# Kernel tuning notes

Measured on AMD Instinct MI355X. Metric: run time of the kernel, lower is better.

The kernel has to match this reference:

```python
import jax, jax.numpy as jnp
import numpy as np

EPS = 1e-8


def normalize_points(p):
    # p: [..., D+1]; normalize feature part to unit L2 norm, fix sign by last coord
    f = p[..., :-1]
    h = p[..., -1:]
    zero_mask = jnp.all(f == 0, axis=-1, keepdims=True)
    f = jnp.where(zero_mask, jnp.ones_like(f), f)
    norm = jnp.linalg.norm(f, axis=-1, keepdims=True)
    nf = f / jnp.clip(norm, EPS)
    n = jnp.concatenate([nf, h], axis=-1)
    sign = jnp.sign(n[..., -1:])
    sign = jnp.where(sign == 0, jnp.ones_like(sign), sign)
    return n * sign


def uhg_transform(x, weight):
    # x: [M, D_in+1], weight: [D_out, D_in]
    f = x[..., :-1]
    h = x[..., -1:]
    t = jnp.matmul(f, weight.T)  # [M, D_out]
    norm = jnp.linalg.norm(t, axis=-1, keepdims=True)
    t = t / jnp.clip(norm, EPS)
    return normalize_points(jnp.concatenate([t, h], axis=-1))


def setup_inputs() -> dict:
    key = jax.random.key(0)
    k1, k2, k3, k4 = jax.random.split(key, 4)
    N, E = 20000, 320000
    D_IN, D_OUT = 256, 256  # in_features-1, out_features
    x = jax.random.normal(k1, (N, D_IN + 1), dtype=jnp.float32)
    edge_index = jax.random.randint(k2, (2, E), 0, N, dtype=jnp.int32)
    # orthogonal-ish init approximated by row-normalized gaussian weights
    W_self = jax.random.normal(k3, (D_OUT, D_IN), dtype=jnp.float32)
    W_self = W_self / jnp.clip(jnp.linalg.norm(W_self, axis=1, keepdims=True), EPS)
    W_neigh = jax.random.normal(k4, (D_OUT, D_IN), dtype=jnp.float32)
    W_neigh = W_neigh / jnp.clip(jnp.linalg.norm(W_neigh, axis=1, keepdims=True), EPS)
    return {"x": x, "W_self": W_self, "W_neigh": W_neigh, "edge_index": edge_index}


def reference(x, W_self, W_neigh, edge_index):
    N = x.shape[0]
    D_OUT = W_self.shape[0]
    x = normalize_points(x)
    row, col = edge_index[0], edge_index[1]

    self_trans = uhg_transform(x, W_self)              # [N, D_OUT+1]
    neigh_trans = uhg_transform(x[col], W_neigh)       # [E, D_OUT+1]

    # mean aggregation: scatter-add full (features + homogeneous), count-divide features only
    out = jnp.zeros((N, D_OUT + 1), dtype=x.dtype).at[:, -1].set(1.0)
    out = out.at[row].add(neigh_trans)
    count = jnp.zeros((N, 1), dtype=x.dtype).at[row].add(1.0)
    count = jnp.clip(count, 1.0)
    out = jnp.concatenate([out[:, :-1] / count, out[:, -1:]], axis=-1)
    out = normalize_points(out)

    # uhg_weighted_average(p1, p2, 0.5): elementwise blend then renormalize
    t = jnp.clip(0.5 / (1.0 - 0.5 + EPS), EPS, 1e8)
    p1 = normalize_points(self_trans)
    p2 = normalize_points(out)
    avg = (p1 * t + p2) / jnp.clip(t + 1.0, EPS)
    combined = normalize_points(avg)
    return normalize_points(combined)
```

## Files before the change

kernel.cpp:

```cpp
#include <hip/hip_runtime.h>
#include <hip/hip_bf16.h>

#define EPSF 1e-8f
#define CAP 64

typedef __attribute__((ext_vector_type(4))) float floatx4;
typedef __attribute__((ext_vector_type(2))) float floatx2;
typedef __attribute__((ext_vector_type(2))) long longx2;

__device__ inline unsigned short f2bf(float v) {
    union { float f; unsigned int u; } un; un.f = v;
    unsigned int r = (un.u + 0x7fffu + ((un.u >> 16) & 1u)) >> 16;
    return (unsigned short)r;
}
__device__ inline float bf2f(unsigned short u) {
    union { unsigned int i; float f; } un; un.i = ((unsigned int)u) << 16;
    return un.f;
}

__device__ inline unsigned char f2fp8(float v) {
#if __has_builtin(__builtin_amdgcn_cvt_pk_fp8_f32)
    return (unsigned char)(__builtin_amdgcn_cvt_pk_fp8_f32(v, 0.f, 0u, false) & 0xff);
#else
    union { float f; unsigned u; } x; x.f = v;
    unsigned s = x.u >> 31; x.u &= 0x7fffffffu;
    if (x.f != x.f || x.f == 0.f) return (unsigned char)(s << 7);
    int e = (int)((x.u >> 23) & 0xff) - 127 + 7;
    unsigned m = x.u & 0x7fffffu;
    unsigned char r;
    if (e >= 1) {
        unsigned keep = m >> 20, rest = m & 0xfffffu;
        keep += (rest > 0x80000u) || (rest == 0x80000u && (keep & 1));
        if (keep == 8) { keep = 0; e += 1; }
        if (e > 15) { e = 15; keep = 6; }
        r = (unsigned char)((e << 3) | keep);
    } else {
        int q = (int)(x.f * 512.f + 0.5f);
        if (q > 7) r = 0x08; else r = (unsigned char)q;
    }
    return (unsigned char)(r | (s << 7));
#endif
}
__device__ inline unsigned pk_fp8x4(float v0, float v1, float v2, float v3) {
#if __has_builtin(__builtin_amdgcn_cvt_pk_fp8_f32)
    unsigned u = __builtin_amdgcn_cvt_pk_fp8_f32(v0, v1, 0u, false);
    u = __builtin_amdgcn_cvt_pk_fp8_f32(v2, v3, u, true);
    return u;
#else
    return (unsigned)f2fp8(v0) | ((unsigned)f2fp8(v1) << 8)
         | ((unsigned)f2fp8(v2) << 16) | ((unsigned)f2fp8(v3) << 24);
#endif
}
__device__ inline floatx2 fp8x2_to_f32(unsigned int u, bool word) {
#if __has_builtin(__builtin_amdgcn_cvt_pk_f32_fp8)
    return word ? __builtin_amdgcn_cvt_pk_f32_fp8(u, true)
                : __builtin_amdgcn_cvt_pk_f32_fp8(u, false);
#else
    floatx2 out;
    #pragma unroll
    for (int i = 0; i < 2; ++i) {
        unsigned char b = (u >> ((word ? 16 : 0) + 8 * i)) & 0xff;
        unsigned s = (b >> 7) & 1, e = (b >> 3) & 15, m = b & 7;
        float v;
        if (e) { union { unsigned u2; float f; } x; x.u2 = (s << 31) | ((e + 120u) << 23) | (m << 20); v = x.f; }
        else   { v = (s ? -1.f : 1.f) * (float)m * 0.001953125f; }
        out[i] = v;
    }
    return out;
#endif
}

__device__ inline void acc16(float* acc, uint4 u) {
    floatx2 p;
    p = fp8x2_to_f32(u.x, false); acc[0]  += p[0]; acc[1]  += p[1];
    p = fp8x2_to_f32(u.x, true);  acc[2]  += p[0]; acc[3]  += p[1];
    p = fp8x2_to_f32(u.y, false); acc[4]  += p[0]; acc[5]  += p[1];
    p = fp8x2_to_f32(u.y, true);  acc[6]  += p[0]; acc[7]  += p[1];
    p = fp8x2_to_f32(u.z, false); acc[8]  += p[0]; acc[9]  += p[1];
    p = fp8x2_to_f32(u.z, true);  acc[10] += p[0]; acc[11] += p[1];
    p = fp8x2_to_f32(u.w, false); acc[12] += p[0]; acc[13] += p[1];
    p = fp8x2_to_f32(u.w, true);  acc[14] += p[0]; acc[15] += p[1];
}

__global__ __launch_bounds__(512) void k_front(
        const float* __restrict__ x, const float* __restrict__ Ws,
        const float* __restrict__ Wn,
        unsigned char* __restrict__ Wswz,
        float* __restrict__ xh, int* __restrict__ cnt, int N) {
    int b = blockIdx.x, t = threadIdx.x;
    if (b < 32) {
        int idx = b * 512 + t;
        int t0 = (idx & 3) * 4;
        int lane = (idx >> 2) & 63;
        int p = (idx >> 8) & 3;
        int g = (idx >> 10) & 3;
        int wq = (idx >> 12) & 3;
        int q = lane >> 4, l16 = lane & 15;
        int row = wq * 64 + g * 16 + l16;
        int s = 2 * p + (t0 >> 3);
        int k0 = 32 * s + 8 * q + (t0 & 7);
        float4 vs = *reinterpret_cast<const float4*>(Ws + row * 256 + k0);
        float4 vn = *reinterpret_cast<const float4*>(Wn + row * 256 + k0);
        reinterpret_cast<unsigned*>(Wswz)[idx] = pk_fp8x4(vs.x, vs.y, vs.z, vs.w);
        reinterpret_cast<unsigned*>(Wswz)[16384 + idx] = pk_fp8x4(vn.x, vn.y, vn.z, vn.w);
    } else {
        int i = (b - 32) * 512 + t;
        if (i < N) {
            xh[i] = fabsf(x[(size_t)i * 257 + 256]);
            cnt[i] = 0;
        }
    }
}

__global__ __launch_bounds__(512, 8) void k_mid(
        const float* __restrict__ x,
        const unsigned char* __restrict__ Wswz,
        const int* __restrict__ ei,
        int* __restrict__ cnt, int* __restrict__ scol,
        unsigned short* __restrict__ selfb, unsigned char* __restrict__ yb8,
        int N, int E, int EB) {
    __shared__ __align__(16) unsigned char As[32][256];
    __shared__ __align__(16) unsigned short sOut[32][256];
    __shared__ float pss[8][32];
    __shared__ float sgnS[32];
    int b = blockIdx.x, tid = threadIdx.x;
    int T = gridDim.x;

    int ebBefore = (int)(((long)b * EB) / T);
    bool isBucket = ((int)(((long)(b + 1) * EB) / T)) != ebBefore;
    if (isBucket) {
        int e = ebBefore * 512 + tid;
        if (e < E) {
            int r = ei[e], c = ei[E + e];
            int pos = atomicAdd(&cnt[r], 1);
            if (pos < CAP) scol[r * CAP + pos] = c;
        }
        return;
    }

    int wave = tid >> 6, lane = tid & 63;
    int quad = lane >> 4, l16 = lane & 15;
    int mat = wave >> 2, wq = wave & 3;
    int row0 = (b - ebBefore) * 32;

    if (tid < 32) {
        int gr = row0 + tid; if (gr >= N) gr = N - 1;
        float h = x[(size_t)gr * 257 + 256];
        sgnS[tid] = (h < 0.f) ? -1.f : 1.f;
    }
    __syncthreads();

    #pragma unroll
    for (int ps = 0; ps < 4; ++ps) {
        int c = ps * 512 + tid;
        int row = c >> 6, k0 = (c & 63) * 4;
        int gr = row0 + row; if (gr >= N) gr = N - 1;
        float4 v = *reinterpret_cast<const float4*>(x + (size_t)gr * 257 + k0);
        float sg = sgnS[row];
        int s = k0 >> 5, q = (k0 >> 3) & 3, j0 = k0 & 7;
        int dst = (q * 64 + (s >> 1) * 16 + (s & 1) * 8 + j0 + row * 16) & 255;
        *reinterpret_cast<unsigned*>(&As[row][dst]) =
            pk_fp8x4(v.x * sg, v.y * sg, v.z * sg, v.w * sg);
    }
    __syncthreads();

    const unsigned char* Wb = Wswz + ((size_t)mat << 16) + ((size_t)wq << 14);
    int rowA = l16, rowB = 16 + l16;

    floatx4 acc[2][4];
    #pragma unroll
    for (int rt = 0; rt < 2; ++rt)
        #pragma unroll
        for (int g = 0; g < 4; ++g) acc[rt][g] = floatx4{0.f, 0.f, 0.f, 0.f};

    #pragma unroll
    for (int p = 0; p < 4; ++p) {
        longx2 a0 = *reinterpret_cast<const longx2*>(
            &As[rowA][(quad * 64 + p * 16 + rowA * 16) & 255]);
        longx2 a1 = *reinterpret_cast<const longx2*>(
            &As[rowB][(quad * 64 + p * 16 + rowB * 16) & 255]);
        #pragma unroll
        for (int g = 0; g < 4; ++g) {
            longx2 w = *reinterpret_cast<const longx2*>(
                Wb + (((g * 4 + p) * 64 + lane) << 4));
            acc[0][g] = __builtin_amdgcn_mfma_f32_16x16x32_fp8_fp8(a0[0], w[0], acc[0][g], 0, 0, 0);
            acc[1][g] = __builtin_amdgcn_mfma_f32_16x16x32_fp8_fp8(a1[0], w[0], acc[1][g], 0, 0, 0);
            acc[0][g] = __builtin_amdgcn_mfma_f32_16x16x32_fp8_fp8(a0[1], w[1], acc[0][g], 0, 0, 0);
            acc[1][g] = __builtin_amdgcn_mfma_f32_16x16x32_fp8_fp8(a1[1], w[1], acc[1][g], 0, 0, 0);
        }
    }

    #pragma unroll
    for (int rt = 0; rt < 2; ++rt) {
        float s[4];
        #pragma unroll
        for (int reg = 0; reg < 4; ++reg) {
            float v = 0.f;
            #pragma unroll
            for (int g = 0; g < 4; ++g) v += acc[rt][g][reg] * acc[rt][g][reg];
            #pragma unroll
            for (int o = 8; o > 0; o >>= 1) v += __shfl_down(v, o, 64);
            s[reg] = v;
        }
        if (l16 == 0) {
            #pragma unroll
            for (int reg = 0; reg < 4; ++reg)
                pss[wave][rt * 16 + quad * 4 + reg] = s[reg];
        }
    }
    __syncthreads();

    int wb = mat * 4;
    #pragma unroll
    for (int rt = 0; rt < 2; ++rt)
        #pragma unroll
        for (int reg = 0; reg < 4; ++reg) {
            int r32 = rt * 16 + quad * 4 + reg;
            float ss = pss[wb][r32] + pss[wb + 1][r32]
                     + pss[wb + 2][r32] + pss[wb + 3][r32];
            bool zero = (ss == 0.f);
            float scale = zero ? 0.f : (1.f / fmaxf(sqrtf(ss), EPSF));
            int xb = ((r32 >> 2) & 3) << 4;
            #pragma unroll
            for (int g = 0; g < 4; ++g) {
                int col = wq * 64 + 16 * g + l16;
                float val = zero ? 0.0625f : acc[rt][g][reg] * scale;
                int cs = col ^ xb;
                if (mat == 0) sOut[r32][cs] = f2bf(val);
                else          As[r32][cs]   = f2fp8(val);
            }
        }
    __syncthreads();

    {
        int r = tid >> 4;
        int gr = row0 + r;
        if (gr < N) {
            int blk = (tid & 15) ^ ((r >> 2) & 3);
            int cb  = blk * 16;
            int cbo = (tid & 15) * 16;
            uint4 a0 = *reinterpret_cast<const uint4*>(&sOut[r][cb]);
            uint4 a1 = *reinterpret_cast<const uint4*>(&sOut[r][cb + 8]);
            *reinterpret_cast<uint4*>(selfb + (size_t)gr * 256 + cbo) = a0;
            *reinterpret_cast<uint4*>(selfb + (size_t)gr * 256 + cbo + 8) = a1;
            uint4 y0 = *reinterpret_cast<const uint4*>(&As[r][cb]);
            *reinterpret_cast<uint4*>(yb8 + (size_t)gr * 256 + cbo) = y0;
        }
    }
}

__global__ __launch_bounds__(256) void k_agg_combine(
        const int* __restrict__ cnt, const int* __restrict__ scol,
        const unsigned char* __restrict__ yb8,
        const float* __restrict__ xh,
        const unsigned short* __restrict__ selfb,
        float* __restrict__ out, int N) {
    int wid = (blockIdx.x * 256 + threadIdx.x) >> 6;
    if (wid >= N) return;
    int lane = threadIdx.x & 63;
    int g = lane >> 4, l16 = lane & 15;
    int deg = cnt[wid]; if (deg > CAP) deg = CAP;
    int beg = wid * CAP;

    float acc[16];
    #pragma unroll
    for (int j = 0; j < 16; ++j) acc[j] = 0.f;

    int e = 0;
    for (; e + 8 <= deg; e += 8) {
        int c0 = scol[beg + e + g];
        int c1 = scol[beg + e + 4 + g];
        uint4 u0 = *reinterpret_cast<const uint4*>(yb8 + (size_t)c0 * 256 + l16 * 16);
        uint4 u1 = *reinterpret_cast<const uint4*>(yb8 + (size_t)c1 * 256 + l16 * 16);
        acc16(acc, u0);
        acc16(acc, u1);
    }
    if (e < deg) {
        int i0 = e + g;
        if (i0 < deg) {
            int c = scol[beg + i0];
            uint4 u = *reinterpret_cast<const uint4*>(yb8 + (size_t)c * 256 + l16 * 16);
            acc16(acc, u);
        }
        int i1 = e + 4 + g;
        if (i1 < deg) {
            int c = scol[beg + i1];
            uint4 u = *reinterpret_cast<const uint4*>(yb8 + (size_t)c * 256 + l16 * 16);
            acc16(acc, u);
        }
    }
    #pragma unroll
    for (int j = 0; j < 16; ++j) {
        acc[j] += __shfl_xor(acc[j], 16, 64);
        acc[j] += __shfl_xor(acc[j], 32, 64);
    }

    float hs = 0.f;
    for (int j = lane; j < deg; j += 64) hs += xh[scol[beg + j]];
    #pragma unroll
    for (int o = 32; o > 0; o >>= 1) hs += __shfl_xor(hs, o, 64);

    float cn = (deg > 0) ? (float)deg : 1.f;
    float rcn = 1.f / cn;
    float m_[16];
    float ss = 0.f;
    #pragma unroll
    for (int j = 0; j < 16; ++j) { m_[j] = acc[j] * rcn; ss += m_[j] * m_[j]; }
    #pragma unroll
    for (int o = 1; o < 16; o <<= 1) ss += __shfl_xor(ss, o, 64);
    bool z = (ss == 0.f);
    float inv = 1.f / fmaxf(z ? 16.f : sqrtf(ss), EPSF);

    const unsigned short* sp = selfb + (size_t)wid * 256 + l16 * 16;
    uint4 s0 = *reinterpret_cast<const uint4*>(sp);
    uint4 s1 = *reinterpret_cast<const uint4*>(sp + 8);
    unsigned sw[8] = { s0.x, s0.y, s0.z, s0.w, s1.x, s1.y, s1.z, s1.w };
    float v_[16];
    float ss2 = 0.f;
    #pragma unroll
    for (int j = 0; j < 8; ++j) {
        float slo = bf2f((unsigned short)(sw[j] & 0xffff));
        float shi = bf2f((unsigned short)(sw[j] >> 16));
        float olo = (z ? 1.f : m_[2 * j]) * inv;
        float ohi = (z ? 1.f : m_[2 * j + 1]) * inv;
        v_[2 * j]     = 0.5f * (slo + olo);
        v_[2 * j + 1] = 0.5f * (shi + ohi);
        ss2 += v_[2 * j] * v_[2 * j] + v_[2 * j + 1] * v_[2 * j + 1];
    }
    #pragma unroll
    for (int o = 1; o < 16; o <<= 1) ss2 += __shfl_xor(ss2, o, 64);
    bool z2 = (ss2 == 0.f);
    float inv2 = 1.f / fmaxf(z2 ? 16.f : sqrtf(ss2), EPSF);

    if (g == 0) {
        float* op = out + (size_t)wid * 257 + l16 * 16;
        #pragma unroll
        for (int j = 0; j < 16; ++j) op[j] = (z2 ? 1.f : v_[j]) * inv2;
    }
    if (lane == 0) out[(size_t)wid * 257 + 256] = 0.5f * (xh[wid] + 1.f + hs);
}

extern "C" void kernel_launch(void* const* d_in, const int* in_sizes, int n_in,
                              void* d_out, int out_size, void* d_ws, size_t ws_size,
                              hipStream_t stream) {
    const float* x  = (const float*)d_in[0];
    const float* Ws = (const float*)d_in[1];
    const float* Wn = (const float*)d_in[2];
    const int*   ei = (const int*)d_in[3];
    int N = in_sizes[0] / 257;
    int E = in_sizes[3] / 2;
    float* out = (float*)d_out;

    char* ws = (char*)d_ws;
    size_t off = 0;
    auto alloc = [&](size_t bytes) {
        void* p = ws + off;
        off = (off + bytes + 255) & ~(size_t)255;
        return p;
    };
    unsigned char* Wswz = (unsigned char*)alloc(131072);
    float* xh    = (float*)alloc((size_t)N * 4);
    unsigned char* yb8 = (unsigned char*)alloc((size_t)N * 256);
    unsigned short* selfb = (unsigned short*)alloc((size_t)N * 256 * 2);
    int* cnt  = (int*)alloc((size_t)N * 4);
    int* scol = (int*)alloc((size_t)N * CAP * 4);

    int XB = (N + 511) / 512;
    hipLaunchKernelGGL(k_front, dim3(32 + XB), dim3(512), 0, stream,
                       x, Ws, Wn, Wswz, xh, cnt, N);
    int GB = (N + 31) / 32, EB = (E + 511) / 512;
    hipLaunchKernelGGL(k_mid, dim3(GB + EB), dim3(512), 0, stream,
                       x, Wswz, ei, cnt, scol, selfb, yb8, N, E, EB);
    hipLaunchKernelGGL(k_agg_combine, dim3((N + 3) / 4), dim3(256), 0, stream,
                       cnt, scol, yb8, xh, selfb, out, N);
}
```

Baseline: 125.6 us.

## Fuse three kernels into one persistent kernel with software grid barriers

```diff
diff --git a/kernel.cpp b/kernel.cpp
--- a/kernel.cpp
+++ b/kernel.cpp
@@ -3,6 +3,7 @@
 
 #define EPSF 1e-8f
 #define CAP 64
+#define NBLK 512
 
 typedef __attribute__((ext_vector_type(4))) float floatx4;
 typedef __attribute__((ext_vector_type(2))) float floatx2;
@@ -82,262 +83,272 @@
     p = fp8x2_to_f32(u.w, true);  acc[14] += p[0]; acc[15] += p[1];
 }
 
-__global__ __launch_bounds__(512) void k_front(
+__device__ inline void swbar(unsigned* bar, unsigned target) {
+    __syncthreads();
+    if (threadIdx.x == 0) {
+        __threadfence();
+        atomicAdd(bar, 1u);
+        long guard = 0;
+        while (atomicAdd(bar, 0u) < target) {
+            __builtin_amdgcn_s_sleep(8);
+            if (++guard > (1L << 22)) break;
+        }
+        __threadfence();
+    }
+    __syncthreads();
+}
+
+__global__ __launch_bounds__(512, 4) void k_fused(
         const float* __restrict__ x, const float* __restrict__ Ws,
-        const float* __restrict__ Wn,
-        unsigned char* __restrict__ Wswz,
-        float* __restrict__ xh, int* __restrict__ cnt, int N) {
-    int b = blockIdx.x, t = threadIdx.x;
-    if (b < 32) {
-        int idx = b * 512 + t;
-        int t0 = (idx & 3) * 4;
-        int lane = (idx >> 2) & 63;
-        int p = (idx >> 8) & 3;
-        int g = (idx >> 10) & 3;
-        int wq = (idx >> 12) & 3;
-        int q = lane >> 4, l16 = lane & 15;
-        int row = wq * 64 + g * 16 + l16;
-        int s = 2 * p + (t0 >> 3);
-        int k0 = 32 * s + 8 * q + (t0 & 7);
-        float4 vs = *reinterpret_cast<const float4*>(Ws + row * 256 + k0);
-        float4 vn = *reinterpret_cast<const float4*>(Wn + row * 256 + k0);
-        reinterpret_cast<unsigned*>(Wswz)[idx] = pk_fp8x4(vs.x, vs.y, vs.z, vs.w);
-        reinterpret_cast<unsigned*>(Wswz)[16384 + idx] = pk_fp8x4(vn.x, vn.y, vn.z, vn.w);
-    } else {
-        int i = (b - 32) * 512 + t;
-        if (i < N) {
-            xh[i] = fabsf(x[(size_t)i * 257 + 256]);
-            cnt[i] = 0;
-        }
-    }
-}
-
-__global__ __launch_bounds__(512, 8) void k_mid(
-        const float* __restrict__ x,
-        const unsigned char* __restrict__ Wswz,
-        const int* __restrict__ ei,
-        int* __restrict__ cnt, int* __restrict__ scol,
+        const float* __restrict__ Wn, const int* __restrict__ ei,
+        unsigned char* __restrict__ Wswz, float* __restrict__ xh,
+        int* __restrict__ cnt, unsigned* __restrict__ bar,
+        int* __restrict__ scol,
         unsigned short* __restrict__ selfb, unsigned char* __restrict__ yb8,
-        int N, int E, int EB) {
+        float* __restrict__ out, int N, int E) {
     __shared__ __align__(16) unsigned char As[32][256];
     __shared__ __align__(16) unsigned short sOut[32][256];
     __shared__ float pss[8][32];
     __shared__ float sgnS[32];
-    int b = blockIdx.x, tid = threadIdx.x;
-    int T = gridDim.x;
-
-    int ebBefore = (int)(((long)b * EB) / T);
-    bool isBucket = ((int)(((long)(b + 1) * EB) / T)) != ebBefore;
-    if (isBucket) {
-        int e = ebBefore * 512 + tid;
-        if (e < E) {
-            int r = ei[e], c = ei[E + e];
-            int pos = atomicAdd(&cnt[r], 1);
-            if (pos < CAP) scol[r * CAP + pos] = c;
-        }
-        return;
-    }
-
+
+    int b0 = blockIdx.x, tid = threadIdx.x;
     int wave = tid >> 6, lane = tid & 63;
     int quad = lane >> 4, l16 = lane & 15;
-    int mat = wave >> 2, wq = wave & 3;
-    int row0 = (b - ebBefore) * 32;
-
-    if (tid < 32) {
-        int gr = row0 + tid; if (gr >= N) gr = N - 1;
-        float h = x[(size_t)gr * 257 + 256];
-        sgnS[tid] = (h < 0.f) ? -1.f : 1.f;
-    }
-    __syncthreads();
-
-    #pragma unroll
-    for (int ps = 0; ps < 4; ++ps) {
-        int c = ps * 512 + tid;
-        int row = c >> 6, k0 = (c & 63) * 4;
-        int gr = row0 + row; if (gr >= N) gr = N - 1;
-        float4 v = *reinterpret_cast<const float4*>(x + (size_t)gr * 257 + k0);
-        float sg = sgnS[row];
-        int s = k0 >> 5, q = (k0 >> 3) & 3, j0 = k0 & 7;
-        int dst = (q * 64 + (s >> 1) * 16 + (s & 1) * 8 + j0 + row * 16) & 255;
-        *reinterpret_cast<unsigned*>(&As[row][dst]) =
-            pk_fp8x4(v.x * sg, v.y * sg, v.z * sg, v.w * sg);
-    }
-    __syncthreads();
-
-    const unsigned char* Wb = Wswz + ((size_t)mat << 16) + ((size_t)wq << 14);
-    int rowA = l16, rowB = 16 + l16;
-
-    floatx4 acc[2][4];
-    #pragma unroll
-    for (int rt = 0; rt < 2; ++rt)
-        #pragma unroll
-        for (int g = 0; g < 4; ++g) acc[rt][g] = floatx4{0.f, 0.f, 0.f, 0.f};
-
-    #pragma unroll
-    for (int p = 0; p < 4; ++p) {
-        longx2 a0 = *reinterpret_cast<const longx2*>(
-            &As[rowA][(quad * 64 + p * 16 + rowA * 16) & 255]);
-        longx2 a1 = *reinterpret_cast<const longx2*>(
-            &As[rowB][(quad * 64 + p * 16 + rowB * 16) & 255]);
-        #pragma unroll
-        for (int g = 0; g < 4; ++g) {
-            longx2 w = *reinterpret_cast<const longx2*>(
-                Wb + (((g * 4 + p) * 64 + lane) << 4));
-            acc[0][g] = __builtin_amdgcn_mfma_f32_16x16x32_fp8_fp8(a0[0], w[0], acc[0][g], 0, 0, 0);
-            acc[1][g] = __builtin_amdgcn_mfma_f32_16x16x32_fp8_fp8(a1[0], w[0], acc[1][g], 0, 0, 0);
-            acc[0][g] = __builtin_amdgcn_mfma_f32_16x16x32_fp8_fp8(a0[1], w[1], acc[0][g], 0, 0, 0);
-            acc[1][g] = __builtin_amdgcn_mfma_f32_16x16x32_fp8_fp8(a1[1], w[1], acc[1][g], 0, 0, 0);
-        }
-    }
-
-    #pragma unroll
-    for (int rt = 0; rt < 2; ++rt) {
-        float s[4];
-        #pragma unroll
-        for (int reg = 0; reg < 4; ++reg) {
-            float v = 0.f;
-            #pragma unroll
-            for (int g = 0; g < 4; ++g) v += acc[rt][g][reg] * acc[rt][g][reg];
-            #pragma unroll
-            for (int o = 8; o > 0; o >>= 1) v += __shfl_down(v, o, 64);
-            s[reg] = v;
-        }
-        if (l16 == 0) {
-            #pragma unroll
-            for (int reg = 0; reg < 4; ++reg)
-                pss[wave][rt * 16 + quad * 4 + reg] = s[reg];
-        }
-    }
-    __syncthreads();
-
-    int wb = mat * 4;
-    #pragma unroll
-    for (int rt = 0; rt < 2; ++rt)
-        #pragma unroll
-        for (int reg = 0; reg < 4; ++reg) {
-            int r32 = rt * 16 + quad * 4 + reg;
-            float ss = pss[wb][r32] + pss[wb + 1][r32]
-                     + pss[wb + 2][r32] + pss[wb + 3][r32];
-            bool zero = (ss == 0.f);
-            float scale = zero ? 0.f : (1.f / fmaxf(sqrtf(ss), EPSF));
-            int xb = ((r32 >> 2) & 3) << 4;
-            #pragma unroll
-            for (int g = 0; g < 4; ++g) {
-                int col = wq * 64 + 16 * g + l16;
-                float val = zero ? 0.0625f : acc[rt][g][reg] * scale;
-                int cs = col ^ xb;
-                if (mat == 0) sOut[r32][cs] = f2bf(val);
-                else          As[r32][cs]   = f2fp8(val);
-            }
-        }
-    __syncthreads();
-
-    {
-        int r = tid >> 4;
-        int gr = row0 + r;
-        if (gr < N) {
-            int blk = (tid & 15) ^ ((r >> 2) & 3);
-            int cb  = blk * 16;
-            int cbo = (tid & 15) * 16;
-            uint4 a0 = *reinterpret_cast<const uint4*>(&sOut[r][cb]);
-            uint4 a1 = *reinterpret_cast<const uint4*>(&sOut[r][cb + 8]);
-            *reinterpret_cast<uint4*>(selfb + (size_t)gr * 256 + cbo) = a0;
-            *reinterpret_cast<uint4*>(selfb + (size_t)gr * 256 + cbo + 8) = a1;
-            uint4 y0 = *reinterpret_cast<const uint4*>(&As[r][cb]);
-            *reinterpret_cast<uint4*>(yb8 + (size_t)gr * 256 + cbo) = y0;
-        }
-    }
-}
-
-__global__ __launch_bounds__(256) void k_agg_combine(
-        const int* __restrict__ cnt, const int* __restrict__ scol,
-        const unsigned char* __restrict__ yb8,
-        const float* __restrict__ xh,
-        const unsigned short* __restrict__ selfb,
-        float* __restrict__ out, int N) {
-    int wid = (blockIdx.x * 256 + threadIdx.x) >> 6;
-    if (wid >= N) return;
-    int lane = threadIdx.x & 63;
-    int g = lane >> 4, l16 = lane & 15;
-    int deg = cnt[wid]; if (deg > CAP) deg = CAP;
-    int beg = wid * CAP;
-
-    float acc[16];
-    #pragma unroll
-    for (int j = 0; j < 16; ++j) acc[j] = 0.f;
-
-    int e = 0;
-    for (; e + 8 <= deg; e += 8) {
-        int c0 = scol[beg + e + g];
-        int c1 = scol[beg + e + 4 + g];
-        uint4 u0 = *reinterpret_cast<const uint4*>(yb8 + (size_t)c0 * 256 + l16 * 16);
-        uint4 u1 = *reinterpret_cast<const uint4*>(yb8 + (size_t)c1 * 256 + l16 * 16);
-        acc16(acc, u0);
-        acc16(acc, u1);
-    }
-    if (e < deg) {
-        int i0 = e + g;
-        if (i0 < deg) {
-            int c = scol[beg + i0];
-            uint4 u = *reinterpret_cast<const uint4*>(yb8 + (size_t)c * 256 + l16 * 16);
-            acc16(acc, u);
-        }
-        int i1 = e + 4 + g;
-        if (i1 < deg) {
-            int c = scol[beg + i1];
-            uint4 u = *reinterpret_cast<const uint4*>(yb8 + (size_t)c * 256 + l16 * 16);
-            acc16(acc, u);
-        }
-    }
-    #pragma unroll
-    for (int j = 0; j < 16; ++j) {
-        acc[j] += __shfl_xor(acc[j], 16, 64);
-        acc[j] += __shfl_xor(acc[j], 32, 64);
-    }
-
-    float hs = 0.f;
-    for (int j = lane; j < deg; j += 64) hs += xh[scol[beg + j]];
-    #pragma unroll
-    for (int o = 32; o > 0; o >>= 1) hs += __shfl_xor(hs, o, 64);
-
-    float cn = (deg > 0) ? (float)deg : 1.f;
-    float rcn = 1.f / cn;
-    float m_[16];
-    float ss = 0.f;
-    #pragma unroll
-    for (int j = 0; j < 16; ++j) { m_[j] = acc[j] * rcn; ss += m_[j] * m_[j]; }
-    #pragma unroll
-    for (int o = 1; o < 16; o <<= 1) ss += __shfl_xor(ss, o, 64);
-    bool z = (ss == 0.f);
-    float inv = 1.f / fmaxf(z ? 16.f : sqrtf(ss), EPSF);
-
-    const unsigned short* sp = selfb + (size_t)wid * 256 + l16 * 16;
-    uint4 s0 = *reinterpret_cast<const uint4*>(sp);
-    uint4 s1 = *reinterpret_cast<const uint4*>(sp + 8);
-    unsigned sw[8] = { s0.x, s0.y, s0.z, s0.w, s1.x, s1.y, s1.z, s1.w };
-    float v_[16];
-    float ss2 = 0.f;
-    #pragma unroll
-    for (int j = 0; j < 8; ++j) {
-        float slo = bf2f((unsigned short)(sw[j] & 0xffff));
-        float shi = bf2f((unsigned short)(sw[j] >> 16));
-        float olo = (z ? 1.f : m_[2 * j]) * inv;
-        float ohi = (z ? 1.f : m_[2 * j + 1]) * inv;
-        v_[2 * j]     = 0.5f * (slo + olo);
-        v_[2 * j + 1] = 0.5f * (shi + ohi);
-        ss2 += v_[2 * j] * v_[2 * j] + v_[2 * j + 1] * v_[2 * j + 1];
-    }
-    #pragma unroll
-    for (int o = 1; o < 16; o <<= 1) ss2 += __shfl_xor(ss2, o, 64);
-    bool z2 = (ss2 == 0.f);
-    float inv2 = 1.f / fmaxf(z2 ? 16.f : sqrtf(ss2), EPSF);
-
-    if (g == 0) {
-        float* op = out + (size_t)wid * 257 + l16 * 16;
-        #pragma unroll
-        for (int j = 0; j < 16; ++j) op[j] = (z2 ? 1.f : v_[j]) * inv2;
-    }
-    if (lane == 0) out[(size_t)wid * 257 + 256] = 0.5f * (xh[wid] + 1.f + hs);
+
+    int XB = (N + 511) >> 9;
+    for (int u = b0; u < 32 + XB; u += NBLK) {
+        if (u < 32) {
+            int idx = u * 512 + tid;
+            int t0 = (idx & 3) * 4;
+            int ln = (idx >> 2) & 63;
+            int p  = (idx >> 8) & 3;
+            int g  = (idx >> 10) & 3;
+            int wq = (idx >> 12) & 3;
+            int q = ln >> 4, m16 = ln & 15;
+            int row = wq * 64 + g * 16 + m16;
+            int s = 2 * p + (t0 >> 3);
+            int k0 = 32 * s + 8 * q + (t0 & 7);
+            float4 vs = *reinterpret_cast<const float4*>(Ws + row * 256 + k0);
+            float4 vn = *reinterpret_cast<const float4*>(Wn + row * 256 + k0);
+            reinterpret_cast<unsigned*>(Wswz)[idx] = pk_fp8x4(vs.x, vs.y, vs.z, vs.w);
+            reinterpret_cast<unsigned*>(Wswz)[16384 + idx] = pk_fp8x4(vn.x, vn.y, vn.z, vn.w);
+        } else {
+            int i = (u - 32) * 512 + tid;
+            if (i < N) xh[i] = fabsf(x[(size_t)i * 257 + 256]);
+        }
+    }
+    swbar(bar, NBLK);
+
+    int GB = (N + 31) >> 5, EBu = (E + 511) >> 9;
+    int GU = GB + EBu;
+    for (int u = b0; u < GU; u += NBLK) {
+        int ebBefore = (int)(((long)u * EBu) / GU);
+        bool isBucket = ((int)(((long)(u + 1) * EBu) / GU)) != ebBefore;
+        if (isBucket) {
+            int e = ebBefore * 512 + tid;
+            if (e < E) {
+                int r = ei[e], c = ei[E + e];
+                int pos = atomicAdd(&cnt[r], 1);
+                if (pos < CAP) scol[r * CAP + pos] = c;
+            }
+        } else {
+            int mat = wave >> 2, wq = wave & 3;
+            int row0 = (u - ebBefore) * 32;
+
+            if (tid < 32) {
+                int gr = row0 + tid; if (gr >= N) gr = N - 1;
+                float h = x[(size_t)gr * 257 + 256];
+                sgnS[tid] = (h < 0.f) ? -1.f : 1.f;
+            }
+            __syncthreads();
+
+            #pragma unroll
+            for (int ps = 0; ps < 4; ++ps) {
+                int c = ps * 512 + tid;
+                int row = c >> 6, k0 = (c & 63) * 4;
+                int gr = row0 + row; if (gr >= N) gr = N - 1;
+                float4 v = *reinterpret_cast<const float4*>(x + (size_t)gr * 257 + k0);
+                float sg = sgnS[row];
+                int s = k0 >> 5, q = (k0 >> 3) & 3, j0 = k0 & 7;
+                int dst = (q * 64 + (s >> 1) * 16 + (s & 1) * 8 + j0 + row * 16) & 255;
+                *reinterpret_cast<unsigned*>(&As[row][dst]) =
+                    pk_fp8x4(v.x * sg, v.y * sg, v.z * sg, v.w * sg);
+            }
+            __syncthreads();
+
+            const unsigned char* Wb = Wswz + ((size_t)mat << 16) + ((size_t)wq << 14);
+            int rowA = l16, rowB = 16 + l16;
+
+            floatx4 acc[2][4];
+            #pragma unroll
+            for (int rt = 0; rt < 2; ++rt)
+                #pragma unroll
+                for (int g = 0; g < 4; ++g) acc[rt][g] = floatx4{0.f, 0.f, 0.f, 0.f};
+
+            #pragma unroll
+            for (int p = 0; p < 4; ++p) {
+                longx2 a0 = *reinterpret_cast<const longx2*>(
+                    &As[rowA][(quad * 64 + p * 16 + rowA * 16) & 255]);
+                longx2 a1 = *reinterpret_cast<const longx2*>(
+                    &As[rowB][(quad * 64 + p * 16 + rowB * 16) & 255]);
+                #pragma unroll
+                for (int g = 0; g < 4; ++g) {
+                    longx2 w = *reinterpret_cast<const longx2*>(
+                        Wb + (((g * 4 + p) * 64 + lane) << 4));
+                    acc[0][g] = __builtin_amdgcn_mfma_f32_16x16x32_fp8_fp8(a0[0], w[0], acc[0][g], 0, 0, 0);
+                    acc[1][g] = __builtin_amdgcn_mfma_f32_16x16x32_fp8_fp8(a1[0], w[0], acc[1][g], 0, 0, 0);
+                    acc[0][g] = __builtin_amdgcn_mfma_f32_16x16x32_fp8_fp8(a0[1], w[1], acc[0][g], 0, 0, 0);
+                    acc[1][g] = __builtin_amdgcn_mfma_f32_16x16x32_fp8_fp8(a1[1], w[1], acc[1][g], 0, 0, 0);
+                }
+            }
+
+            #pragma unroll
+            for (int rt = 0; rt < 2; ++rt) {
+                float s[4];
+                #pragma unroll
+                for (int reg = 0; reg < 4; ++reg) {
+                    float v = 0.f;
+                    #pragma unroll
+                    for (int g = 0; g < 4; ++g) v += acc[rt][g][reg] * acc[rt][g][reg];
+                    #pragma unroll
+                    for (int o = 8; o > 0; o >>= 1) v += __shfl_down(v, o, 64);
+                    s[reg] = v;
+                }
+                if (l16 == 0) {
+                    #pragma unroll
+                    for (int reg = 0; reg < 4; ++reg)
+                        pss[wave][rt * 16 + quad * 4 + reg] = s[reg];
+                }
+            }
+            __syncthreads();
+
+            int wb = mat * 4;
+            #pragma unroll
+            for (int rt = 0; rt < 2; ++rt)
+                #pragma unroll
+                for (int reg = 0; reg < 4; ++reg) {
+                    int r32 = rt * 16 + quad * 4 + reg;
+                    float ss = pss[wb][r32] + pss[wb + 1][r32]
+                             + pss[wb + 2][r32] + pss[wb + 3][r32];
+                    bool zero = (ss == 0.f);
+                    float scale = zero ? 0.f : (1.f / fmaxf(sqrtf(ss), EPSF));
+                    int xb = ((r32 >> 2) & 3) << 4;
+                    #pragma unroll
+                    for (int g = 0; g < 4; ++g) {
+                        int col = wq * 64 + 16 * g + l16;
+                        float val = zero ? 0.0625f : acc[rt][g][reg] * scale;
+                        int cs = col ^ xb;
+                        if (mat == 0) sOut[r32][cs] = f2bf(val);
+                        else          As[r32][cs]   = f2fp8(val);
+                    }
+                }
+            __syncthreads();
+
+            {
+                int r = tid >> 4;
+                int gr = row0 + r;
+                if (gr < N) {
+                    int blk = (tid & 15) ^ ((r >> 2) & 3);
+                    int cb  = blk * 16;
+                    int cbo = (tid & 15) * 16;
+                    uint4 a0 = *reinterpret_cast<const uint4*>(&sOut[r][cb]);
+                    uint4 a1 = *reinterpret_cast<const uint4*>(&sOut[r][cb + 8]);
+                    *reinterpret_cast<uint4*>(selfb + (size_t)gr * 256 + cbo) = a0;
+                    *reinterpret_cast<uint4*>(selfb + (size_t)gr * 256 + cbo + 8) = a1;
+                    uint4 y0 = *reinterpret_cast<const uint4*>(&As[r][cb]);
+                    *reinterpret_cast<uint4*>(yb8 + (size_t)gr * 256 + cbo) = y0;
+                }
+            }
+        }
+        __syncthreads();
+    }
+    swbar(bar, 2u * NBLK);
+
+    int g = quad;
+    int AU = (N + 7) >> 3;
+    for (int u = b0; u < AU; u += NBLK) {
+        int wid = u * 8 + wave;
+        if (wid >= N) continue;
+        int deg = cnt[wid]; if (deg > CAP) deg = CAP;
+        int beg = wid * CAP;
+
+        float acc[16];
+        #pragma unroll
+        for (int j = 0; j < 16; ++j) acc[j] = 0.f;
+
+        int e = 0;
+        for (; e + 8 <= deg; e += 8) {
+            int c0 = scol[beg + e + g];
+            int c1 = scol[beg + e + 4 + g];
+            uint4 u0 = *reinterpret_cast<const uint4*>(yb8 + (size_t)c0 * 256 + l16 * 16);
+            uint4 u1 = *reinterpret_cast<const uint4*>(yb8 + (size_t)c1 * 256 + l16 * 16);
+            acc16(acc, u0);
+            acc16(acc, u1);
+        }
+        if (e < deg) {
+            int i0 = e + g;
+            if (i0 < deg) {
+                int c = scol[beg + i0];
+                uint4 uu = *reinterpret_cast<const uint4*>(yb8 + (size_t)c * 256 + l16 * 16);
+                acc16(acc, uu);
+            }
+            int i1 = e + 4 + g;
+            if (i1 < deg) {
+                int c = scol[beg + i1];
+                uint4 uu = *reinterpret_cast<const uint4*>(yb8 + (size_t)c * 256 + l16 * 16);
+                acc16(acc, uu);
+            }
+        }
+        #pragma unroll
+        for (int j = 0; j < 16; ++j) {
+            acc[j] += __shfl_xor(acc[j], 16, 64);
+            acc[j] += __shfl_xor(acc[j], 32, 64);
+        }
+
+        float hs = 0.f;
+        for (int j = lane; j < deg; j += 64) hs += xh[scol[beg + j]];
+        #pragma unroll
+        for (int o = 32; o > 0; o >>= 1) hs += __shfl_xor(hs, o, 64);
+
+        float cn = (deg > 0) ? (float)deg : 1.f;
+        float rcn = 1.f / cn;
+        float m_[16];
+        float ss = 0.f;
+        #pragma unroll
+        for (int j = 0; j < 16; ++j) { m_[j] = acc[j] * rcn; ss += m_[j] * m_[j]; }
+        #pragma unroll
+        for (int o = 1; o < 16; o <<= 1) ss += __shfl_xor(ss, o, 64);
+        bool z = (ss == 0.f);
+        float inv = 1.f / fmaxf(z ? 16.f : sqrtf(ss), EPSF);
+
+        const unsigned short* sp = selfb + (size_t)wid * 256 + l16 * 16;
+        uint4 s0 = *reinterpret_cast<const uint4*>(sp);
+        uint4 s1 = *reinterpret_cast<const uint4*>(sp + 8);
+        unsigned sw[8] = { s0.x, s0.y, s0.z, s0.w, s1.x, s1.y, s1.z, s1.w };
+        float v_[16];
+        float ss2 = 0.f;
+        #pragma unroll
+        for (int j = 0; j < 8; ++j) {
+            float slo = bf2f((unsigned short)(sw[j] & 0xffff));
+            float shi = bf2f((unsigned short)(sw[j] >> 16));
+            float olo = (z ? 1.f : m_[2 * j]) * inv;
+            float ohi = (z ? 1.f : m_[2 * j + 1]) * inv;
+            v_[2 * j]     = 0.5f * (slo + olo);
+            v_[2 * j + 1] = 0.5f * (shi + ohi);
+            ss2 += v_[2 * j] * v_[2 * j] + v_[2 * j + 1] * v_[2 * j + 1];
+        }
+        #pragma unroll
+        for (int o = 1; o < 16; o <<= 1) ss2 += __shfl_xor(ss2, o, 64);
+        bool z2 = (ss2 == 0.f);
+        float inv2 = 1.f / fmaxf(z2 ? 16.f : sqrtf(ss2), EPSF);
+
+        if (g == 0) {
+            float* op = out + (size_t)wid * 257 + l16 * 16;
+            #pragma unroll
+            for (int j = 0; j < 16; ++j) op[j] = (z2 ? 1.f : v_[j]) * inv2;
+        }
+        if (lane == 0) out[(size_t)wid * 257 + 256] = 0.5f * (xh[wid] + 1.f + hs);
+    }
 }
 
 extern "C" void kernel_launch(void* const* d_in, const int* in_sizes, int n_in,
@@ -363,14 +374,13 @@
     unsigned char* yb8 = (unsigned char*)alloc((size_t)N * 256);
     unsigned short* selfb = (unsigned short*)alloc((size_t)N * 256 * 2);
     int* cnt  = (int*)alloc((size_t)N * 4);
-    int* scol = (int*)alloc((size_t)N * CAP * 4);
-
-    int XB = (N + 511) / 512;
-    hipLaunchKernelGGL(k_front, dim3(32 + XB), dim3(512), 0, stream,
-                       x, Ws, Wn, Wswz, xh, cnt, N);
-    int GB = (N + 31) / 32, EB = (E + 511) / 512;
-    hipLaunchKernelGGL(k_mid, dim3(GB + EB), dim3(512), 0, stream,
-                       x, Wswz, ei, cnt, scol, selfb, yb8, N, E, EB);
-    hipLaunchKernelGGL(k_agg_combine, dim3((N + 3) / 4), dim3(256), 0, stream,
-                       cnt, scol, yb8, xh, selfb, out, N);
-}
+    unsigned* bar = (unsigned*)alloc(256);
+    int* scol = (int*)alloc((size_t)E ? (size_t)N * CAP * 4 : 0);
+
+    size_t zbytes = (size_t)((char*)bar + 256 - (char*)cnt);
+    hipMemsetAsync(cnt, 0, zbytes, stream);
+
+    hipLaunchKernelGGL(k_fused, dim3(NBLK), dim3(512), 0, stream,
+                       x, Ws, Wn, ei, Wswz, xh, cnt, bar, scol,
+                       selfb, yb8, out, N, E);
+}
```

Measured after the change: 228.9 us. 1.82x slower.

## Write GEMM outputs directly to global and fuse homogeneous sum into gather loop

Applied to the files above, without the earlier changes.

```diff
diff --git a/kernel.cpp b/kernel.cpp
--- a/kernel.cpp
+++ b/kernel.cpp
@@ -120,7 +120,6 @@
         unsigned short* __restrict__ selfb, unsigned char* __restrict__ yb8,
         int N, int E, int EB) {
     __shared__ __align__(16) unsigned char As[32][256];
-    __shared__ __align__(16) unsigned short sOut[32][256];
     __shared__ float pss[8][32];
     __shared__ float sgnS[32];
     int b = blockIdx.x, tid = threadIdx.x;
@@ -216,37 +215,20 @@
         #pragma unroll
         for (int reg = 0; reg < 4; ++reg) {
             int r32 = rt * 16 + quad * 4 + reg;
+            int gr = row0 + r32;
+            if (gr >= N) continue;
             float ss = pss[wb][r32] + pss[wb + 1][r32]
                      + pss[wb + 2][r32] + pss[wb + 3][r32];
             bool zero = (ss == 0.f);
             float scale = zero ? 0.f : (1.f / fmaxf(sqrtf(ss), EPSF));
-            int xb = ((r32 >> 2) & 3) << 4;
             #pragma unroll
             for (int g = 0; g < 4; ++g) {
                 int col = wq * 64 + 16 * g + l16;
                 float val = zero ? 0.0625f : acc[rt][g][reg] * scale;
-                int cs = col ^ xb;
-                if (mat == 0) sOut[r32][cs] = f2bf(val);
-                else          As[r32][cs]   = f2fp8(val);
+                if (mat == 0) selfb[(size_t)gr * 256 + col] = f2bf(val);
+                else          yb8[(size_t)gr * 256 + col] = f2fp8(val);
             }
         }
-    __syncthreads();
-
-    {
-        int r = tid >> 4;
-        int gr = row0 + r;
-        if (gr < N) {
-            int blk = (tid & 15) ^ ((r >> 2) & 3);
-            int cb  = blk * 16;
-            int cbo = (tid & 15) * 16;
-            uint4 a0 = *reinterpret_cast<const uint4*>(&sOut[r][cb]);
-            uint4 a1 = *reinterpret_cast<const uint4*>(&sOut[r][cb + 8]);
-            *reinterpret_cast<uint4*>(selfb + (size_t)gr * 256 + cbo) = a0;
-            *reinterpret_cast<uint4*>(selfb + (size_t)gr * 256 + cbo + 8) = a1;
-            uint4 y0 = *reinterpret_cast<const uint4*>(&As[r][cb]);
-            *reinterpret_cast<uint4*>(yb8 + (size_t)gr * 256 + cbo) = y0;
-        }
-    }
 }
 
 __global__ __launch_bounds__(256) void k_agg_combine(
@@ -265,40 +247,42 @@
     float acc[16];
     #pragma unroll
     for (int j = 0; j < 16; ++j) acc[j] = 0.f;
+    float hq = 0.f;
 
     int e = 0;
-    for (; e + 8 <= deg; e += 8) {
+    for (; e + 16 <= deg; e += 16) {
         int c0 = scol[beg + e + g];
         int c1 = scol[beg + e + 4 + g];
+        int c2 = scol[beg + e + 8 + g];
+        int c3 = scol[beg + e + 12 + g];
         uint4 u0 = *reinterpret_cast<const uint4*>(yb8 + (size_t)c0 * 256 + l16 * 16);
         uint4 u1 = *reinterpret_cast<const uint4*>(yb8 + (size_t)c1 * 256 + l16 * 16);
+        uint4 u2 = *reinterpret_cast<const uint4*>(yb8 + (size_t)c2 * 256 + l16 * 16);
+        uint4 u3 = *reinterpret_cast<const uint4*>(yb8 + (size_t)c3 * 256 + l16 * 16);
+        hq += xh[c0] + xh[c1] + xh[c2] + xh[c3];
+        acc16(acc, u0); acc16(acc, u1); acc16(acc, u2); acc16(acc, u3);
+    }
+    for (; e + 4 <= deg; e += 4) {
+        int c0 = scol[beg + e + g];
+        uint4 u0 = *reinterpret_cast<const uint4*>(yb8 + (size_t)c0 * 256 + l16 * 16);
+        hq += xh[c0];
         acc16(acc, u0);
-        acc16(acc, u1);
-    }
-    if (e < deg) {
-        int i0 = e + g;
-        if (i0 < deg) {
-            int c = scol[beg + i0];
-            uint4 u = *reinterpret_cast<const uint4*>(yb8 + (size_t)c * 256 + l16 * 16);
-            acc16(acc, u);
-        }
-        int i1 = e + 4 + g;
-        if (i1 < deg) {
-            int c = scol[beg + i1];
-            uint4 u = *reinterpret_cast<const uint4*>(yb8 + (size_t)c * 256 + l16 * 16);
-            acc16(acc, u);
-        }
+    }
+    int rem = deg - e;
+    if (g < rem) {
+        int c0 = scol[beg + e + g];
+        uint4 u0 = *reinterpret_cast<const uint4*>(yb8 + (size_t)c0 * 256 + l16 * 16);
+        hq += xh[c0];
+        acc16(acc, u0);
     }
     #pragma unroll
     for (int j = 0; j < 16; ++j) {
         acc[j] += __shfl_xor(acc[j], 16, 64);
         acc[j] += __shfl_xor(acc[j], 32, 64);
     }
-
-    float hs = 0.f;
-    for (int j = lane; j < deg; j += 64) hs += xh[scol[beg + j]];
-    #pragma unroll
-    for (int o = 32; o > 0; o >>= 1) hs += __shfl_xor(hs, o, 64);
+    hq += __shfl_xor(hq, 16, 64);
+    hq += __shfl_xor(hq, 32, 64);
+    float hs = hq;
 
     float cn = (deg > 0) ? (float)deg : 1.f;
     float rcn = 1.f / cn;
```

After: 127.4 us. Within noise of the previous version (+1.4%).
